# Kernel tuning notes

Measured on AMD Instinct MI355X. Metric: run time of the kernel, lower is better.

## Reference

```python
import jax, jax.numpy as jnp
import numpy as np

B, D, G, H = 65536, 512, 16, 128


def setup_inputs() -> dict:
    key = jax.random.key(0)
    ks = jax.random.split(key, 8)
    s = 1.0 / np.sqrt(D)
    sh = 1.0 / np.sqrt(H)
    return {
        "z": jax.random.normal(ks[0], (B, D), dtype=jnp.float32),
        "Wc": jax.random.uniform(ks[1], (D, G), jnp.float32, -s, s),
        "bc": jax.random.uniform(ks[2], (G,), jnp.float32, -s, s),
        "W1": jax.random.uniform(ks[3], (G, D, H), jnp.float32, -s, s),
        "b1": jax.random.uniform(ks[4], (G, H), jnp.float32, -s, s),
        "W2": jax.random.uniform(ks[5], (G, H), jnp.float32, -sh, sh),
        "b2": jax.random.uniform(ks[6], (G,), jnp.float32, -sh, sh),
    }


def reference(z, Wc, bc, W1, b1, W2, b2):
    # classifier head + softmax
    logits = z @ Wc + bc                                  # [B, G]
    p_g = jax.nn.softmax(logits, axis=1)                  # [B, G]
    # G experts fused as one batched GEMM: fc1 -> GELU -> fc2 (dropout = identity at eval)
    h = jax.nn.gelu(jnp.einsum('bd,gdh->bgh', z, W1) + b1, approximate=False)  # [B, G, H]
    y_all = jnp.einsum('bgh,gh->bg', h, W2) + b2          # [B, G]
    return logits, p_g, y_all
```

## Files before the change

### kernel.cpp

```cpp
#include <hip/hip_runtime.h>
#include <cstdint>
#include <cstddef>

typedef __bf16 bf16x8 __attribute__((ext_vector_type(8)));
typedef float f32x4 __attribute__((ext_vector_type(4)));
typedef unsigned short ushortx8 __attribute__((ext_vector_type(8)));
typedef unsigned short ushortx4 __attribute__((ext_vector_type(4)));

__device__ __forceinline__ unsigned short f2bf(float f) {
  union { float f; unsigned int u; } v; v.f = f;
  return (unsigned short)((v.u + 0x8000u) >> 16);
}

__device__ __forceinline__ float gelu_s(float x) {
  float x2 = x * x;
  float p = __builtin_fmaf(x2, -0.10294324f, -2.30220819f);
  float e = __builtin_amdgcn_exp2f(x * p);
  return x * __builtin_amdgcn_rcpf(1.0f + e);
}

#define GLOAD16(gsrc, ldst)                                                  \
  __builtin_amdgcn_global_load_lds(                                          \
      (const __attribute__((address_space(1))) unsigned int*)(gsrc),         \
      (__attribute__((address_space(3))) unsigned int*)(uintptr_t)(          \
          (char*)(ldst)),                                                    \
      16, 0, 0)

#define SWZ_FRAG(base, R, C8)                                                \
  (*(const bf16x8*)((base) + (((R) >> 5) * 4096) +                           \
                    ((((R)&31) * 8 + ((C8) ^ ((R)&7))) * 16)))

__global__ __launch_bounds__(256) void k_convert(
    const float* __restrict__ z, const float* __restrict__ W1,
    const float* __restrict__ Wc, unsigned short* __restrict__ zb,
    unsigned short* __restrict__ w1t, unsigned short* __restrict__ wct) {
  int bid = blockIdx.x;
  int tid = threadIdx.x;
  if (bid < 8192) {
    const float4* z4 = (const float4*)z;
    size_t base = (size_t)bid * 1024 + tid;
#pragma unroll
    for (int it = 0; it < 4; ++it) {
      size_t i4 = base + (size_t)it * 256;
      float4 a = z4[i4];
      ushortx4 r;
      r[0] = f2bf(a.x); r[1] = f2bf(a.y); r[2] = f2bf(a.z); r[3] = f2bf(a.w);
      *(ushortx4*)(zb + i4 * 4) = r;
    }
  } else if (bid < 8192 + 1024) {
    __shared__ float tile[32][33];
    int b = bid - 8192;
    int gg = b >> 6;
    int t = b & 63;
    int d0 = (t >> 2) * 32;
    int h0 = (t & 3) * 32;
    int tx = tid & 31, ty = tid >> 5;
#pragma unroll
    for (int r = 0; r < 4; ++r) {
      int d = d0 + r * 8 + ty;
      tile[r * 8 + ty][tx] = W1[(gg << 16) + d * 128 + h0 + tx];
    }
    __syncthreads();
#pragma unroll
    for (int r = 0; r < 4; ++r) {
      int h = h0 + r * 8 + ty;
      w1t[(gg << 16) + h * 512 + d0 + tx] = f2bf(tile[tx][r * 8 + ty]);
    }
  } else {
#pragma unroll
    for (int j = 0; j < 32; ++j) {
      int i = j * 256 + tid;
      wct[(i & 15) * 512 + (i >> 4)] = f2bf(Wc[i]);
    }
  }
}

__global__ __launch_bounds__(256, 4) void k_main(
    const unsigned short* __restrict__ zb,
    const unsigned short* __restrict__ w1t,
    const unsigned short* __restrict__ wct,
    const float* __restrict__ bc, const float* __restrict__ b1,
    const float* __restrict__ w2, const float* __restrict__ b2,
    float* __restrict__ out) {
  __shared__ alignas(16) char lds[16384 + 16384 + 1024];
  const int tid = threadIdx.x;
  const int wq = tid >> 6;
  const int ln = tid & 63;
  const int l15 = ln & 15;
  const int l4 = ln >> 4;
  const int c8s = (((tid & 7) ^ ((tid >> 3) & 7))) * 8;
  char* ldsB = lds + 16384;

  if (blockIdx.x >= 512) {
    const int eb = blockIdx.x - 512;
    const int idx = (eb & 7) * 1024 + (eb >> 3);
    const int e = idx & 15;
    const int mbase = (idx >> 4) * 128;
    const unsigned short* ag = zb + (size_t)(mbase + (tid >> 3)) * 512 + c8s;
    const unsigned short* bg =
        w1t + e * 65536 + (tid >> 3) * 512 + c8s;
    const int wr = wq >> 1;
    const int wc = wq & 1;
    f32x4 acc[4][4] = {};
    for (int kt = 0; kt < 8; ++kt) {
      const int ko = kt * 64;
#pragma unroll
      for (int it = 0; it < 4; ++it)
        GLOAD16(ag + it * 32 * 512 + ko, lds + it * 4096 + tid * 16);
#pragma unroll
      for (int it = 0; it < 4; ++it)
        GLOAD16(bg + it * 32 * 512 + ko, ldsB + it * 4096 + tid * 16);
      __syncthreads();
#pragma unroll
      for (int ks = 0; ks < 2; ++ks) {
        bf16x8 af[4];
#pragma unroll
        for (int rt = 0; rt < 4; ++rt)
          af[rt] = SWZ_FRAG(lds, wr * 64 + rt * 16 + l15, ks * 4 + l4);
#pragma unroll
        for (int ct = 0; ct < 4; ++ct) {
          bf16x8 bfv = SWZ_FRAG(ldsB, wc * 64 + ct * 16 + l15, ks * 4 + l4);
#pragma unroll
          for (int rt = 0; rt < 4; ++rt)
            acc[rt][ct] = __builtin_amdgcn_mfma_f32_16x16x32_bf16(
                af[rt], bfv, acc[rt][ct], 0, 0, 0);
        }
      }
      __syncthreads();
    }
    float b1v[4], w2v[4];
#pragma unroll
    for (int ct = 0; ct < 4; ++ct) {
      int n = wc * 64 + ct * 16 + l15;
      b1v[ct] = b1[e * 128 + n];
      w2v[ct] = w2[e * 128 + n];
    }
    float* ylds = (float*)(lds + 32768);
#pragma unroll
    for (int rt = 0; rt < 4; ++rt) {
#pragma unroll
      for (int i = 0; i < 4; ++i) {
        float s = 0.0f;
#pragma unroll
        for (int ct = 0; ct < 4; ++ct)
          s += gelu_s(acc[rt][ct][i] + b1v[ct]) * w2v[ct];
#pragma unroll
        for (int off = 1; off < 16; off <<= 1)
          s += __shfl_xor(s, off, 16);
        if (l15 == 0) ylds[wq * 64 + rt * 16 + l4 * 4 + i] = s;
      }
    }
    __syncthreads();
    if (tid < 128) {
      int rl = tid & 63, half = tid >> 6;
      float y = ylds[half * 128 + rl] + ylds[half * 128 + 64 + rl] + b2[e];
      out[(size_t)2097152 + (size_t)(mbase + half * 64 + rl) * 16 + e] = y;
    }
  } else {
    const int mbase = blockIdx.x * 128;
    const unsigned short* ag = zb + (size_t)(mbase + (tid >> 3)) * 512 + c8s;
    const unsigned short* wb = wct + l15 * 512 + l4 * 8;
    f32x4 acc2[2] = {};
    for (int kt = 0; kt < 8; ++kt) {
      const int ko = kt * 64;
#pragma unroll
      for (int it = 0; it < 4; ++it)
        GLOAD16(ag + it * 32 * 512 + ko, lds + it * 4096 + tid * 16);
      bf16x8 bfr0 = *(const bf16x8*)(wb + ko);
      bf16x8 bfr1 = *(const bf16x8*)(wb + ko + 32);
      __syncthreads();
#pragma unroll
      for (int rt = 0; rt < 2; ++rt) {
        bf16x8 a0 = SWZ_FRAG(lds, wq * 32 + rt * 16 + l15, l4);
        acc2[rt] = __builtin_amdgcn_mfma_f32_16x16x32_bf16(a0, bfr0, acc2[rt],
                                                           0, 0, 0);
        bf16x8 a1 = SWZ_FRAG(lds, wq * 32 + rt * 16 + l15, 4 + l4);
        acc2[rt] = __builtin_amdgcn_mfma_f32_16x16x32_bf16(a1, bfr1, acc2[rt],
                                                           0, 0, 0);
      }
      __syncthreads();
    }
    float bcv = bc[l15];
#pragma unroll
    for (int rt = 0; rt < 2; ++rt) {
#pragma unroll
      for (int i = 0; i < 4; ++i) {
        int row = wq * 32 + rt * 16 + l4 * 4 + i;
        float lg = acc2[rt][i] + bcv;
        float mx = lg;
#pragma unroll
        for (int off = 1; off < 16; off <<= 1)
          mx = fmaxf(mx, __shfl_xor(mx, off, 16));
        float ex = __expf(lg - mx);
        float sm = ex;
#pragma unroll
        for (int off = 1; off < 16; off <<= 1)
          sm += __shfl_xor(sm, off, 16);
        size_t ro = (size_t)(mbase + row) * 16 + l15;
        out[ro] = lg;
        out[1048576 + ro] = ex / sm;
      }
    }
  }
}

extern "C" void kernel_launch(void* const* d_in, const int* in_sizes, int n_in,
                              void* d_out, int out_size, void* d_ws,
                              size_t ws_size, hipStream_t stream) {
  const float* z = (const float*)d_in[0];
  const float* Wc = (const float*)d_in[1];
  const float* bc = (const float*)d_in[2];
  const float* W1 = (const float*)d_in[3];
  const float* b1 = (const float*)d_in[4];
  const float* W2 = (const float*)d_in[5];
  const float* b2 = (const float*)d_in[6];
  float* out = (float*)d_out;

  unsigned short* zb = (unsigned short*)d_ws;
  unsigned short* w1t = zb + (size_t)65536 * 512;
  unsigned short* wct = w1t + (size_t)16 * 128 * 512;

  k_convert<<<8192 + 1024 + 1, 256, 0, stream>>>(z, W1, Wc, zb, w1t, wct);
  k_main<<<512 + 8192, 256, 0, stream>>>(zb, w1t, wct, bc, b1, W2, b2, out);
}
```

Baseline: 375.6 us.

## Fuse convert and main kernels into persistent cooperative kernel with atomic tile scheduler

Replaces the two-launch sequence (bf16 conversion, then GEMM/epilogue) with a single persistent cooperative kernel. The grid converts z, W1 and Wc, passes a grid-wide sync, then pulls logits and expert tiles from per-XCD atomic counters so each XCD works on a contiguous range of rows. The aim is to remove the second launch and the tail between kernels, and to improve L2 reuse of z rows across experts. The trade-offs are a grid barrier, an atomic fetch per tile, and fewer resident blocks than the original large grid, which may reduce latency hiding. The old two-kernel path is kept as a fallback.

```diff
diff --git a/kernel.cpp b/kernel.cpp
--- a/kernel.cpp
+++ b/kernel.cpp
@@ -1,10 +1,12 @@
 #include <hip/hip_runtime.h>
+#include <hip/hip_cooperative_groups.h>
 #include <cstdint>
 #include <cstddef>
 
+namespace cg = cooperative_groups;
+
 typedef __bf16 bf16x8 __attribute__((ext_vector_type(8)));
 typedef float f32x4 __attribute__((ext_vector_type(4)));
-typedef unsigned short ushortx8 __attribute__((ext_vector_type(8)));
 typedef unsigned short ushortx4 __attribute__((ext_vector_type(4)));
 
 __device__ __forceinline__ unsigned short f2bf(float f) {
@@ -29,6 +31,200 @@
 #define SWZ_FRAG(base, R, C8)                                                \
   (*(const bf16x8*)((base) + (((R) >> 5) * 4096) +                           \
                     ((((R)&31) * 8 + ((C8) ^ ((R)&7))) * 16)))
+
+__device__ __forceinline__ void expert_tile(
+    int e, int mbase, const unsigned short* __restrict__ zb,
+    const unsigned short* __restrict__ w1t, const float* __restrict__ b1,
+    const float* __restrict__ w2, const float* __restrict__ b2,
+    float* __restrict__ out, char* lds, int tid, int wq, int l15, int l4,
+    int c8s) {
+  char* ldsB = lds + 16384;
+  const unsigned short* ag = zb + (size_t)(mbase + (tid >> 3)) * 512 + c8s;
+  const unsigned short* bg = w1t + e * 65536 + (tid >> 3) * 512 + c8s;
+  const int wr = wq >> 1;
+  const int wc = wq & 1;
+  f32x4 acc[4][4] = {};
+  for (int kt = 0; kt < 8; ++kt) {
+    const int ko = kt * 64;
+#pragma unroll
+    for (int it = 0; it < 4; ++it)
+      GLOAD16(ag + it * 32 * 512 + ko, lds + it * 4096 + tid * 16);
+#pragma unroll
+    for (int it = 0; it < 4; ++it)
+      GLOAD16(bg + it * 32 * 512 + ko, ldsB + it * 4096 + tid * 16);
+    __syncthreads();
+#pragma unroll
+    for (int ks = 0; ks < 2; ++ks) {
+      bf16x8 af[4];
+#pragma unroll
+      for (int rt = 0; rt < 4; ++rt)
+        af[rt] = SWZ_FRAG(lds, wr * 64 + rt * 16 + l15, ks * 4 + l4);
+#pragma unroll
+      for (int ct = 0; ct < 4; ++ct) {
+        bf16x8 bfv = SWZ_FRAG(ldsB, wc * 64 + ct * 16 + l15, ks * 4 + l4);
+#pragma unroll
+        for (int rt = 0; rt < 4; ++rt)
+          acc[rt][ct] = __builtin_amdgcn_mfma_f32_16x16x32_bf16(
+              af[rt], bfv, acc[rt][ct], 0, 0, 0);
+      }
+    }
+    __syncthreads();
+  }
+  float b1v[4], w2v[4];
+#pragma unroll
+  for (int ct = 0; ct < 4; ++ct) {
+    int n = wc * 64 + ct * 16 + l15;
+    b1v[ct] = b1[e * 128 + n];
+    w2v[ct] = w2[e * 128 + n];
+  }
+  float* ylds = (float*)(lds + 32768);
+#pragma unroll
+  for (int rt = 0; rt < 4; ++rt) {
+#pragma unroll
+    for (int i = 0; i < 4; ++i) {
+      float s = 0.0f;
+#pragma unroll
+      for (int ct = 0; ct < 4; ++ct)
+        s += gelu_s(acc[rt][ct][i] + b1v[ct]) * w2v[ct];
+#pragma unroll
+      for (int off = 1; off < 16; off <<= 1) s += __shfl_xor(s, off, 16);
+      if (l15 == 0) ylds[wq * 64 + rt * 16 + l4 * 4 + i] = s;
+    }
+  }
+  __syncthreads();
+  if (tid < 128) {
+    int rl = tid & 63, half = tid >> 6;
+    float y = ylds[half * 128 + rl] + ylds[half * 128 + 64 + rl] + b2[e];
+    out[(size_t)2097152 + (size_t)(mbase + half * 64 + rl) * 16 + e] = y;
+  }
+}
+
+__device__ __forceinline__ void logits_tile(
+    int mbase, const unsigned short* __restrict__ zb,
+    const unsigned short* __restrict__ wct, const float* __restrict__ bc,
+    float* __restrict__ out, char* lds, int tid, int wq, int l15, int l4,
+    int c8s) {
+  const unsigned short* ag = zb + (size_t)(mbase + (tid >> 3)) * 512 + c8s;
+  const unsigned short* wb = wct + l15 * 512 + l4 * 8;
+  f32x4 acc2[2] = {};
+  for (int kt = 0; kt < 8; ++kt) {
+    const int ko = kt * 64;
+#pragma unroll
+    for (int it = 0; it < 4; ++it)
+      GLOAD16(ag + it * 32 * 512 + ko, lds + it * 4096 + tid * 16);
+    bf16x8 bfr0 = *(const bf16x8*)(wb + ko);
+    bf16x8 bfr1 = *(const bf16x8*)(wb + ko + 32);
+    __syncthreads();
+#pragma unroll
+    for (int rt = 0; rt < 2; ++rt) {
+      bf16x8 a0 = SWZ_FRAG(lds, wq * 32 + rt * 16 + l15, l4);
+      acc2[rt] =
+          __builtin_amdgcn_mfma_f32_16x16x32_bf16(a0, bfr0, acc2[rt], 0, 0, 0);
+      bf16x8 a1 = SWZ_FRAG(lds, wq * 32 + rt * 16 + l15, 4 + l4);
+      acc2[rt] =
+          __builtin_amdgcn_mfma_f32_16x16x32_bf16(a1, bfr1, acc2[rt], 0, 0, 0);
+    }
+    __syncthreads();
+  }
+  float bcv = bc[l15];
+#pragma unroll
+  for (int rt = 0; rt < 2; ++rt) {
+#pragma unroll
+    for (int i = 0; i < 4; ++i) {
+      int row = wq * 32 + rt * 16 + l4 * 4 + i;
+      float lg = acc2[rt][i] + bcv;
+      float mx = lg;
+#pragma unroll
+      for (int off = 1; off < 16; off <<= 1)
+        mx = fmaxf(mx, __shfl_xor(mx, off, 16));
+      float ex = __expf(lg - mx);
+      float sm = ex;
+#pragma unroll
+      for (int off = 1; off < 16; off <<= 1) sm += __shfl_xor(sm, off, 16);
+      size_t ro = (size_t)(mbase + row) * 16 + l15;
+      out[ro] = lg;
+      out[1048576 + ro] = ex / sm;
+    }
+  }
+}
+
+__global__ __launch_bounds__(256, 4) void k_fused(
+    const float* __restrict__ z, const float* __restrict__ W1,
+    const float* __restrict__ Wc, const float* __restrict__ bc,
+    const float* __restrict__ b1, const float* __restrict__ w2,
+    const float* __restrict__ b2, unsigned short* __restrict__ zb,
+    unsigned short* __restrict__ w1t, unsigned short* __restrict__ wct,
+    int* __restrict__ cnt, float* __restrict__ out) {
+  __shared__ alignas(16) char lds[33792];
+  __shared__ int s_t;
+  const int NB = gridDim.x;
+  const int b = blockIdx.x;
+  const int tid = threadIdx.x;
+  const int wq = tid >> 6;
+  const int l15 = tid & 15;
+  const int l4 = (tid >> 4) & 3;
+  const int c8s = (((tid & 7) ^ ((tid >> 3) & 7))) * 8;
+  const int xcd = b & 7;
+  const int slot = b >> 3;
+  const int SX = NB >> 3;
+
+  {
+    const float4* z4 = (const float4*)z;
+    for (int c = slot; c < 1024; c += SX) {
+      size_t base = ((size_t)xcd * 1024 + c) * 1024 + tid;
+#pragma unroll
+      for (int it = 0; it < 4; ++it) {
+        size_t i4 = base + (size_t)it * 256;
+        float4 a = z4[i4];
+        ushortx4 r;
+        r[0] = f2bf(a.x); r[1] = f2bf(a.y); r[2] = f2bf(a.z); r[3] = f2bf(a.w);
+        *(ushortx4*)(zb + i4 * 4) = r;
+      }
+    }
+  }
+  for (int w = b; w < 1024; w += NB) {
+    float* tile = (float*)lds;
+    int gg = w >> 6;
+    int t6 = w & 63;
+    int d0 = (t6 >> 2) * 32;
+    int h0 = (t6 & 3) * 32;
+    int tx = tid & 31, ty = tid >> 5;
+#pragma unroll
+    for (int r = 0; r < 4; ++r)
+      tile[(r * 8 + ty) * 33 + tx] =
+          W1[(gg << 16) + (d0 + r * 8 + ty) * 128 + h0 + tx];
+    __syncthreads();
+#pragma unroll
+    for (int r = 0; r < 4; ++r)
+      w1t[(gg << 16) + (h0 + r * 8 + ty) * 512 + d0 + tx] =
+          f2bf(tile[tx * 33 + r * 8 + ty]);
+    __syncthreads();
+  }
+  if (b < 32) {
+    int i = b * 256 + tid;
+    wct[(i & 15) * 512 + (i >> 4)] = f2bf(Wc[i]);
+  }
+  if (b == NB - 1 && tid < 8) atomicExch(&cnt[tid], 0);
+
+  __threadfence();
+  cg::this_grid().sync();
+  __threadfence();
+
+  while (true) {
+    if (tid == 0) s_t = atomicAdd(&cnt[xcd], 1);
+    __syncthreads();
+    int t = s_t;
+    if (t >= 1088) break;
+    int g = t / 17;
+    int r = t - g * 17;
+    int mbase = (xcd * 64 + g) * 128;
+    if (r == 0)
+      logits_tile(mbase, zb, wct, bc, out, lds, tid, wq, l15, l4, c8s);
+    else
+      expert_tile(r - 1, mbase, zb, w1t, b1, w2, b2, out, lds, tid, wq, l15,
+                  l4, c8s);
+  }
+}
 
 __global__ __launch_bounds__(256) void k_convert(
     const float* __restrict__ z, const float* __restrict__ W1,
@@ -56,16 +252,13 @@
     int h0 = (t & 3) * 32;
     int tx = tid & 31, ty = tid >> 5;
 #pragma unroll
-    for (int r = 0; r < 4; ++r) {
-      int d = d0 + r * 8 + ty;
-      tile[r * 8 + ty][tx] = W1[(gg << 16) + d * 128 + h0 + tx];
-    }
-    __syncthreads();
-#pragma unroll
-    for (int r = 0; r < 4; ++r) {
-      int h = h0 + r * 8 + ty;
-      w1t[(gg << 16) + h * 512 + d0 + tx] = f2bf(tile[tx][r * 8 + ty]);
-    }
+    for (int r = 0; r < 4; ++r)
+      tile[r * 8 + ty][tx] = W1[(gg << 16) + (d0 + r * 8 + ty) * 128 + h0 + tx];
+    __syncthreads();
+#pragma unroll
+    for (int r = 0; r < 4; ++r)
+      w1t[(gg << 16) + (h0 + r * 8 + ty) * 512 + d0 + tx] =
+          f2bf(tile[tx][r * 8 + ty]);
   } else {
 #pragma unroll
     for (int j = 0; j < 32; ++j) {
@@ -78,129 +271,23 @@
 __global__ __launch_bounds__(256, 4) void k_main(
     const unsigned short* __restrict__ zb,
     const unsigned short* __restrict__ w1t,
-    const unsigned short* __restrict__ wct,
-    const float* __restrict__ bc, const float* __restrict__ b1,
-    const float* __restrict__ w2, const float* __restrict__ b2,
-    float* __restrict__ out) {
-  __shared__ alignas(16) char lds[16384 + 16384 + 1024];
+    const unsigned short* __restrict__ wct, const float* __restrict__ bc,
+    const float* __restrict__ b1, const float* __restrict__ w2,
+    const float* __restrict__ b2, float* __restrict__ out) {
+  __shared__ alignas(16) char lds[33792];
   const int tid = threadIdx.x;
   const int wq = tid >> 6;
-  const int ln = tid & 63;
-  const int l15 = ln & 15;
-  const int l4 = ln >> 4;
+  const int l15 = tid & 15;
+  const int l4 = (tid >> 4) & 3;
   const int c8s = (((tid & 7) ^ ((tid >> 3) & 7))) * 8;
-  char* ldsB = lds + 16384;
-
   if (blockIdx.x >= 512) {
     const int eb = blockIdx.x - 512;
     const int idx = (eb & 7) * 1024 + (eb >> 3);
-    const int e = idx & 15;
-    const int mbase = (idx >> 4) * 128;
-    const unsigned short* ag = zb + (size_t)(mbase + (tid >> 3)) * 512 + c8s;
-    const unsigned short* bg =
-        w1t + e * 65536 + (tid >> 3) * 512 + c8s;
-    const int wr = wq >> 1;
-    const int wc = wq & 1;
-    f32x4 acc[4][4] = {};
-    for (int kt = 0; kt < 8; ++kt) {
-      const int ko = kt * 64;
-#pragma unroll
-      for (int it = 0; it < 4; ++it)
-        GLOAD16(ag + it * 32 * 512 + ko, lds + it * 4096 + tid * 16);
-#pragma unroll
-      for (int it = 0; it < 4; ++it)
-        GLOAD16(bg + it * 32 * 512 + ko, ldsB + it * 4096 + tid * 16);
-      __syncthreads();
-#pragma unroll
-      for (int ks = 0; ks < 2; ++ks) {
-        bf16x8 af[4];
-#pragma unroll
-        for (int rt = 0; rt < 4; ++rt)
-          af[rt] = SWZ_FRAG(lds, wr * 64 + rt * 16 + l15, ks * 4 + l4);
-#pragma unroll
-        for (int ct = 0; ct < 4; ++ct) {
-          bf16x8 bfv = SWZ_FRAG(ldsB, wc * 64 + ct * 16 + l15, ks * 4 + l4);
-#pragma unroll
-          for (int rt = 0; rt < 4; ++rt)
-            acc[rt][ct] = __builtin_amdgcn_mfma_f32_16x16x32_bf16(
-                af[rt], bfv, acc[rt][ct], 0, 0, 0);
-        }
-      }
-      __syncthreads();
-    }
-    float b1v[4], w2v[4];
-#pragma unroll
-    for (int ct = 0; ct < 4; ++ct) {
-      int n = wc * 64 + ct * 16 + l15;
-      b1v[ct] = b1[e * 128 + n];
-      w2v[ct] = w2[e * 128 + n];
-    }
-    float* ylds = (float*)(lds + 32768);
-#pragma unroll
-    for (int rt = 0; rt < 4; ++rt) {
-#pragma unroll
-      for (int i = 0; i < 4; ++i) {
-        float s = 0.0f;
-#pragma unroll
-        for (int ct = 0; ct < 4; ++ct)
-          s += gelu_s(acc[rt][ct][i] + b1v[ct]) * w2v[ct];
-#pragma unroll
-        for (int off = 1; off < 16; off <<= 1)
-          s += __shfl_xor(s, off, 16);
-        if (l15 == 0) ylds[wq * 64 + rt * 16 + l4 * 4 + i] = s;
-      }
-    }
-    __syncthreads();
-    if (tid < 128) {
-      int rl = tid & 63, half = tid >> 6;
-      float y = ylds[half * 128 + rl] + ylds[half * 128 + 64 + rl] + b2[e];
-      out[(size_t)2097152 + (size_t)(mbase + half * 64 + rl) * 16 + e] = y;
-    }
+    expert_tile(idx & 15, (idx >> 4) * 128, zb, w1t, b1, w2, b2, out, lds, tid,
+                wq, l15, l4, c8s);
   } else {
-    const int mbase = blockIdx.x * 128;
-    const unsigned short* ag = zb + (size_t)(mbase + (tid >> 3)) * 512 + c8s;
-    const unsigned short* wb = wct + l15 * 512 + l4 * 8;
-    f32x4 acc2[2] = {};
-    for (int kt = 0; kt < 8; ++kt) {
-      const int ko = kt * 64;
-#pragma unroll
-      for (int it = 0; it < 4; ++it)
-        GLOAD16(ag + it * 32 * 512 + ko, lds + it * 4096 + tid * 16);
-      bf16x8 bfr0 = *(const bf16x8*)(wb + ko);
-      bf16x8 bfr1 = *(const bf16x8*)(wb + ko + 32);
-      __syncthreads();
-#pragma unroll
-      for (int rt = 0; rt < 2; ++rt) {
-        bf16x8 a0 = SWZ_FRAG(lds, wq * 32 + rt * 16 + l15, l4);
-        acc2[rt] = __builtin_amdgcn_mfma_f32_16x16x32_bf16(a0, bfr0, acc2[rt],
-                                                           0, 0, 0);
-        bf16x8 a1 = SWZ_FRAG(lds, wq * 32 + rt * 16 + l15, 4 + l4);
-        acc2[rt] = __builtin_amdgcn_mfma_f32_16x16x32_bf16(a1, bfr1, acc2[rt],
-                                                           0, 0, 0);
-      }
-      __syncthreads();
-    }
-    float bcv = bc[l15];
-#pragma unroll
-    for (int rt = 0; rt < 2; ++rt) {
-#pragma unroll
-      for (int i = 0; i < 4; ++i) {
-        int row = wq * 32 + rt * 16 + l4 * 4 + i;
-        float lg = acc2[rt][i] + bcv;
-        float mx = lg;
-#pragma unroll
-        for (int off = 1; off < 16; off <<= 1)
-          mx = fmaxf(mx, __shfl_xor(mx, off, 16));
-        float ex = __expf(lg - mx);
-        float sm = ex;
-#pragma unroll
-        for (int off = 1; off < 16; off <<= 1)
-          sm += __shfl_xor(sm, off, 16);
-        size_t ro = (size_t)(mbase + row) * 16 + l15;
-        out[ro] = lg;
-        out[1048576 + ro] = ex / sm;
-      }
-    }
+    logits_tile(blockIdx.x * 128, zb, wct, bc, out, lds, tid, wq, l15, l4,
+                c8s);
   }
 }
 
@@ -219,7 +306,29 @@
   unsigned short* zb = (unsigned short*)d_ws;
   unsigned short* w1t = zb + (size_t)65536 * 512;
   unsigned short* wct = w1t + (size_t)16 * 128 * 512;
-
-  k_convert<<<8192 + 1024 + 1, 256, 0, stream>>>(z, W1, Wc, zb, w1t, wct);
-  k_main<<<512 + 8192, 256, 0, stream>>>(zb, w1t, wct, bc, b1, W2, b2, out);
-}
+  int* cnt = (int*)(wct + (size_t)16 * 512);
+
+  int dev = 0;
+  (void)hipGetDevice(&dev);
+  int coop = 0;
+  (void)hipDeviceGetAttribute(&coop, hipDeviceAttributeCooperativeLaunch, dev);
+  int maxb = 0;
+  (void)hipOccupancyMaxActiveBlocksPerMultiprocessor(&maxb, k_fused, 256, 0);
+  int NB = maxb * 256;
+  if (NB > 1024) NB = 1024;
+  NB &= ~7;
+
+  bool ok = false;
+  if (coop && NB >= 64) {
+    void* kargs[] = {(void*)&z,   (void*)&W1,  (void*)&Wc,  (void*)&bc,
+                     (void*)&b1,  (void*)&W2,  (void*)&b2,  (void*)&zb,
+                     (void*)&w1t, (void*)&wct, (void*)&cnt, (void*)&out};
+    hipError_t err = hipLaunchCooperativeKernel(
+        (const void*)k_fused, dim3(NB), dim3(256), kargs, 0, stream);
+    ok = (err == hipSuccess);
+  }
+  if (!ok) {
+    k_convert<<<8192 + 1024 + 1, 256, 0, stream>>>(z, W1, Wc, zb, w1t, wct);
+    k_main<<<512 + 8192, 256, 0, stream>>>(zb, w1t, wct, bc, b1, W2, b2, out);
+  }
+}
```

Result: slower. 696.4 us (+85.4%).
